# Kernel tuning notes

Hardware: AMD Instinct MI355X
Metric: run time of the kernel (lower is better)

Reference implementation:

```python
import jax, jax.numpy as jnp
import numpy as np

N_MEL = 80


def _bce_with_logits(x, t):
    # mean over all elements, numerically stable
    return jnp.mean(jnp.maximum(x, 0.0) - x * t + jnp.log1p(jnp.exp(-jnp.abs(x))))


def _spectral_mel_loss(pred, target):
    w = np.ones(N_MEL, dtype=np.float32)
    w[N_MEL // 4: 3 * N_MEL // 4] *= 1.5
    w[3 * N_MEL // 4:] *= 0.8
    w = jnp.asarray(w)[None, :, None]
    weighted_mse = jnp.mean((pred * w - target * w) ** 2)
    l1 = jnp.mean(jnp.abs(pred - target))
    dp = pred[:, :, 1:] - pred[:, :, :-1]
    dt = target[:, :, 1:] - target[:, :, :-1]
    spectral = jnp.mean((dp - dt) ** 2)
    return weighted_mse + 0.3 * l1 + 0.2 * spectral


def _perceptual_loss(pred, target):
    fw = jnp.exp(-jnp.arange(N_MEL, dtype=jnp.float32) / 20.0)[None, :, None]
    weighted = ((pred - target) ** 2) * fw
    l1 = jnp.mean(jnp.abs(pred - target))
    return jnp.mean(weighted) + 0.5 * l1


def _style_loss(pred, target):
    mean_loss = jnp.mean((jnp.mean(pred, axis=2) - jnp.mean(target, axis=2)) ** 2)
    # torch.var defaults to unbiased (ddof=1)
    var_loss = jnp.mean((jnp.var(pred, axis=2, ddof=1) - jnp.var(target, axis=2, ddof=1)) ** 2)
    c, t = pred.shape[1], pred.shape[2]
    gram_p = jnp.einsum('bct,bdt->bcd', pred, pred) / (c * t)
    gram_t = jnp.einsum('bct,bdt->bcd', target, target) / (c * t)
    gram_loss = jnp.mean((gram_p - gram_t) ** 2)
    return mean_loss + var_loss + 0.5 * gram_loss


def _monotonic_loss(att):
    # att: [B, mel_len, text_len]; vectorized form of the per-step violation loop
    b, mel_len, _ = att.shape
    peaks = jnp.argmax(att, axis=2).astype(jnp.float32)  # [B, mel_len]
    viol = jnp.maximum(peaks[:, :-1] - peaks[:, 1:], 0.0)
    return jnp.sum(viol) / (b * mel_len)


def setup_inputs() -> dict:
    key = jax.random.key(0)
    ks = jax.random.split(key, 6)
    B, C, T, L = 64, N_MEL, 2000, 200
    return {
        'mel_out': jax.random.normal(ks[0], (B, C, T), jnp.float32),
        'mel_out_postnet': jax.random.normal(ks[1], (B, C, T), jnp.float32),
        'mel_target': jax.random.normal(ks[2], (B, C, T), jnp.float32),
        'gate_out': jax.random.normal(ks[3], (B, T), jnp.float32),
        'gate_target': jax.random.uniform(ks[4], (B, T), jnp.float32),
        'attention_weights': jax.random.uniform(ks[5], (B, T, L), jnp.float32),
    }


def reference(mel_out, mel_out_postnet, mel_target, gate_out, gate_target, attention_weights):
    # loss weights (hparams defaults); guide_loss omitted (method truncated in source)
    mel_w, gate_w, spec_w, perc_w, style_w, mono_w = 1.0, 1.0, 0.3, 0.2, 0.1, 0.1
    gate_inner_w = 1.3  # AdaptiveGateLoss initial_weight

    mel_loss = jnp.mean((mel_out - mel_target) ** 2) + jnp.mean((mel_out_postnet - mel_target) ** 2)
    gate_loss = gate_inner_w * _bce_with_logits(gate_out.reshape(-1, 1), gate_target.reshape(-1, 1))
    spectral = _spectral_mel_loss(mel_out_postnet, mel_target)
    perceptual = _perceptual_loss(mel_out_postnet, mel_target)
    style = _style_loss(mel_out_postnet, mel_target)
    mono = _monotonic_loss(attention_weights)

    total = (mel_w * mel_loss + gate_w * gate_loss + spec_w * spectral
             + perc_w * perceptual + style_w * style + mono_w * mono)
    return total
```

## Files before the change

kernel.cpp:

```cpp
#include <hip/hip_runtime.h>
#include <math.h>

#define N_MEL 80
#define B_    64
#define T_    2000
#define L_    200
#define ROWS   (B_*N_MEL)
#define NTOT   (B_*N_MEL*T_)
#define GATE_N (B_*T_)
#define ATT_ROWS (B_*T_)

#define ACC_STRIDE 16
#define ACC_FLOATS 1024
#define VIOL_SLOT  16
#define WS_M8      ACC_FLOATS
#define WS_ROWPART (WS_M8 + 8*64*6400)

typedef __attribute__((ext_vector_type(8)))  short bf16x8;
typedef __attribute__((ext_vector_type(16))) float f32x16;

__device__ __forceinline__ float blockReduceSum256(float v) {
    __shared__ float red[4];
    #pragma unroll
    for (int off = 32; off; off >>= 1) v += __shfl_down(v, off, 64);
    int lane = threadIdx.x & 63, w = threadIdx.x >> 6;
    if (lane == 0) red[w] = v;
    __syncthreads();
    if (threadIdx.x == 0) v = red[0] + red[1] + red[2] + red[3];
    return v;
}

__device__ __forceinline__ unsigned short f2bf(float f) {
    unsigned u = __float_as_uint(f);
    u = (u + 0x7fffu + ((u >> 16) & 1u)) >> 16;
    return (unsigned short)u;
}

__global__ __launch_bounds__(256) void k_melrow(const float* __restrict__ mo,
                                                const float* __restrict__ mp,
                                                const float* __restrict__ mt,
                                                float* __restrict__ rowpart,
                                                float* __restrict__ acc) {
    if (blockIdx.x == 0) {
        *(float4*)(acc + threadIdx.x * 4) = make_float4(0.f, 0.f, 0.f, 0.f);
    }
    const int row = blockIdx.x;
    const long base = (long)row * T_;
    const float4* mo4 = (const float4*)(mo + base);
    const float4* mp4 = (const float4*)(mp + base);
    const float4* mt4 = (const float4*)(mt + base);

    float s1 = 0, s2 = 0, sl1 = 0, std_ = 0, sp = 0, sp2 = 0, st = 0, st2 = 0;
    for (int i = threadIdx.x; i < T_/4; i += 256) {
        float4 a = mo4[i], p = mp4[i], t = mt4[i];
        float e0 = a.x - t.x, e1 = a.y - t.y, e2 = a.z - t.z, e3 = a.w - t.w;
        s1 += e0*e0 + e1*e1 + e2*e2 + e3*e3;
        float d0 = p.x - t.x, d1 = p.y - t.y, d2 = p.z - t.z, d3 = p.w - t.w;
        s2 += d0*d0 + d1*d1 + d2*d2 + d3*d3;
        sl1 += fabsf(d0) + fabsf(d1) + fabsf(d2) + fabsf(d3);
        sp  += p.x + p.y + p.z + p.w;
        sp2 += p.x*p.x + p.y*p.y + p.z*p.z + p.w*p.w;
        st  += t.x + t.y + t.z + t.w;
        st2 += t.x*t.x + t.y*t.y + t.z*t.z + t.w*t.w;
        float q1 = d1 - d0, q2 = d2 - d1, q3 = d3 - d2;
        std_ += q1*q1 + q2*q2 + q3*q3;
        if (i > 0) {
            float dprev = mp[base + 4*i - 1] - mt[base + 4*i - 1];
            float q0 = d0 - dprev;
            std_ += q0*q0;
        }
    }

    __shared__ float red[4][8];
    float vals[8] = {s1, s2, sl1, std_, sp, sp2, st, st2};
    #pragma unroll
    for (int k = 0; k < 8; k++) {
        float v = vals[k];
        #pragma unroll
        for (int off = 32; off; off >>= 1) v += __shfl_down(v, off, 64);
        vals[k] = v;
    }
    int lane = threadIdx.x & 63, w = threadIdx.x >> 6;
    if (lane == 0) {
        #pragma unroll
        for (int k = 0; k < 8; k++) red[w][k] = vals[k];
    }
    __syncthreads();
    if (threadIdx.x == 0) {
        #pragma unroll
        for (int k = 0; k < 8; k++)
            rowpart[row*8 + k] = red[0][k] + red[1][k] + red[2][k] + red[3][k];
    }
}

__global__ __launch_bounds__(256) void k_melred(const float* __restrict__ rowpart,
                                                float* __restrict__ acc) {
    int row = blockIdx.x*256 + threadIdx.x;
    float a[8] = {0,0,0,0,0,0,0,0};
    if (row < ROWS) {
        const float4 lo = *(const float4*)(rowpart + row*8);
        const float4 hi = *(const float4*)(rowpart + row*8 + 4);
        float r0=lo.x, r1=lo.y, r2=lo.z, r3=lo.w, r4=hi.x, r5=hi.y, r6=hi.z, r7=hi.w;
        int c = row % N_MEL;
        float wc = (c >= 3*N_MEL/4) ? 0.8f : ((c >= N_MEL/4) ? 1.5f : 1.0f);
        float fw = expf(-(float)c / 20.0f);
        a[0] = r0;
        a[1] = r1;
        a[2] = wc*wc*r1;
        a[3] = r2;
        a[4] = r3;
        a[5] = fw*r1;
        float md = (r4 - r6) * (1.0f / T_);
        a[6] = md*md;
        float vp = (r5 - r4*r4*(1.0f/T_)) * (1.0f/(T_-1));
        float vt = (r7 - r6*r6*(1.0f/T_)) * (1.0f/(T_-1));
        float vd = vp - vt;
        a[7] = vd*vd;
    }
    __shared__ float red[4][8];
    #pragma unroll
    for (int k = 0; k < 8; k++) {
        float v = a[k];
        #pragma unroll
        for (int off = 32; off; off >>= 1) v += __shfl_down(v, off, 64);
        a[k] = v;
    }
    int lane = threadIdx.x & 63, w = threadIdx.x >> 6;
    if (lane == 0) {
        #pragma unroll
        for (int k = 0; k < 8; k++) red[w][k] = a[k];
    }
    __syncthreads();
    if (threadIdx.x == 0) {
        #pragma unroll
        for (int k = 0; k < 8; k++)
            atomicAdd(&acc[k*ACC_STRIDE], red[0][k] + red[1][k] + red[2][k] + red[3][k]);
    }
}

__global__ __launch_bounds__(256) void k_gate(const float* __restrict__ xp,
                                              const float* __restrict__ tp,
                                              float* __restrict__ acc) {
    const float4* x4 = (const float4*)xp;
    const float4* t4 = (const float4*)tp;
    float s = 0;
    for (int i = blockIdx.x*256 + threadIdx.x; i < GATE_N/4; i += gridDim.x*256) {
        float4 x = x4[i], t = t4[i];
        float xs[4] = {x.x, x.y, x.z, x.w}, ts[4] = {t.x, t.y, t.z, t.w};
        #pragma unroll
        for (int k = 0; k < 4; k++)
            s += fmaxf(xs[k], 0.0f) - xs[k]*ts[k] + log1pf(expf(-fabsf(xs[k])));
    }
    float tot = blockReduceSum256(s);
    if (threadIdx.x == 0) atomicAdd(&acc[8*ACC_STRIDE], tot);
}

#define AV_ROWS 64
__device__ __forceinline__ void scan_sub(const float* __restrict__ rowp, int q,
                                         float& bOut, int& pOut) {
    const float4* rp = (const float4*)rowp;
    float bx=-1.f, by=-1.f, bz=-1.f, bw=-1.f;
    int jx=0, jy=0, jz=0, jw=0;
    const int n = (q < 2) ? 13 : 12;
    #pragma unroll
    for (int i = 0; i < 13; i++) {
        if (i < n) {
            int j = q + 4*i;
            float4 v = rp[j];
            if (v.x > bx) { bx = v.x; jx = j; }
            if (v.y > by) { by = v.y; jy = j; }
            if (v.z > bz) { bz = v.z; jz = j; }
            if (v.w > bw) { bw = v.w; jw = j; }
        }
    }
    float b = bx; int p = 4*jx;
    if (by > b || (by == b && 4*jy+1 < p)) { b = by; p = 4*jy+1; }
    if (bz > b || (bz == b && 4*jz+2 < p)) { b = bz; p = 4*jz+2; }
    if (bw > b || (bw == b && 4*jw+3 < p)) { b = bw; p = 4*jw+3; }
    bOut = b; pOut = p;
}

__device__ __forceinline__ void merge4(float& b, int& p) {
    #pragma unroll
    for (int m = 1; m <= 2; m <<= 1) {
        float ob = __shfl_xor(b, m, 64);
        int   op = __shfl_xor(p, m, 64);
        if (ob > b || (ob == b && op < p)) { b = ob; p = op; }
    }
}

__global__ __launch_bounds__(256) void k_argviol(const float* __restrict__ att,
                                                 float* __restrict__ acc) {
    __shared__ float pk[AV_ROWS + 1];
    const int g = threadIdx.x >> 2;
    const int q = threadIdx.x & 3;
    const int r0 = blockIdx.x * AV_ROWS;
    const int r  = r0 + g;

    float b; int p;
    scan_sub(att + (long)r * L_, q, b, p);
    merge4(b, p);
    if (q == 0) pk[g] = (float)p;

    const int rb = r0 + AV_ROWS;
    const bool need_b = ((rb % T_) != 0) && (rb < ATT_ROWS);
    if (g == 0 && need_b) {
        float b2; int p2;
        scan_sub(att + (long)rb * L_, q, b2, p2);
        merge4(b2, p2);
        if (q == 0) pk[AV_ROWS] = (float)p2;
    }
    __syncthreads();

    float s = 0;
    if (threadIdx.x < AV_ROWS) {
        int rr = r0 + threadIdx.x;
        if (((rr + 1) % T_) != 0)
            s = fmaxf(pk[threadIdx.x] - pk[threadIdx.x + 1], 0.0f);
    }
    float tot = blockReduceSum256(s);
    if (threadIdx.x == 0)
        atomicAdd(&acc[(VIOL_SLOT + (blockIdx.x & 15))*ACC_STRIDE], tot);
}

__global__ __launch_bounds__(192) void k_gram(const float* __restrict__ mp,
                                              const float* __restrict__ mt,
                                              float* __restrict__ M8) {
    const int b  = blockIdx.x >> 3;
    const int kc = blockIdx.x & 7;
    const int k0 = kc * 256;
    const int NS = (kc < 7) ? 16 : 13;

    __shared__ unsigned short Dls[2][96][24];
    __shared__ unsigned short Sls[2][96][24];

    const int tid  = threadIdx.x;
    const int row  = tid >> 1;
    const int half = tid & 1;
    const int lane = tid & 63;
    const int wv   = tid >> 6;
    const long bbase = (long)b * (N_MEL * T_);
    const float* prow = mp + bbase + (long)row * T_ + k0 + half * 8;
    const float* trow = mt + bbase + (long)row * T_ + k0 + half * 8;
    const bool rv = (row < N_MEL);

    f32x16 acc0 = {}, acc1 = {}, acc2 = {};
    float4 pa0, pa1, ta0, ta1;

    auto loadreg = [&](int s) {
        if (rv) {
            pa0 = *(const float4*)(prow + s*16);
            pa1 = *(const float4*)(prow + s*16 + 4);
            ta0 = *(const float4*)(trow + s*16);
            ta1 = *(const float4*)(trow + s*16 + 4);
        } else {
            pa0 = pa1 = ta0 = ta1 = make_float4(0.f, 0.f, 0.f, 0.f);
        }
    };
    auto writelds = [&](int buf) {
        bf16x8 d, s;
        d[0]=f2bf(pa0.x-ta0.x); d[1]=f2bf(pa0.y-ta0.y); d[2]=f2bf(pa0.z-ta0.z); d[3]=f2bf(pa0.w-ta0.w);
        d[4]=f2bf(pa1.x-ta1.x); d[5]=f2bf(pa1.y-ta1.y); d[6]=f2bf(pa1.z-ta1.z); d[7]=f2bf(pa1.w-ta1.w);
        s[0]=f2bf(pa0.x+ta0.x); s[1]=f2bf(pa0.y+ta0.y); s[2]=f2bf(pa0.z+ta0.z); s[3]=f2bf(pa0.w+ta0.w);
        s[4]=f2bf(pa1.x+ta1.x); s[5]=f2bf(pa1.y+ta1.y); s[6]=f2bf(pa1.z+ta1.z); s[7]=f2bf(pa1.w+ta1.w);
        *(bf16x8*)&Dls[buf][row][half*8] = d;
        *(bf16x8*)&Sls[buf][row][half*8] = s;
    };

    loadreg(0);
    writelds(0);
    __syncthreads();

    const int frow = lane & 31;
    const int fkh  = lane >> 5;
    for (int s = 0; s < NS; s++) {
        const int cur = s & 1;
        if (s + 1 < NS) loadreg(s + 1);
        bf16x8 af = *(const bf16x8*)&Dls[cur][wv*32 + frow][fkh*8];
        bf16x8 b0 = *(const bf16x8*)&Sls[cur][      frow][fkh*8];
        bf16x8 b1 = *(const bf16x8*)&Sls[cur][ 32 + frow][fkh*8];
        bf16x8 b2 = *(const bf16x8*)&Sls[cur][ 64 + frow][fkh*8];
        acc0 = __builtin_amdgcn_mfma_f32_32x32x16_bf16(af, b0, acc0, 0, 0, 0);
        acc1 = __builtin_amdgcn_mfma_f32_32x32x16_bf16(af, b1, acc1, 0, 0, 0);
        acc2 = __builtin_amdgcn_mfma_f32_32x32x16_bf16(af, b2, acc2, 0, 0, 0);
        if (s + 1 < NS) writelds((s + 1) & 1);
        __syncthreads();
    }

    float* Mb = M8 + ((long)(kc * B_ + b)) * 6400;
    #pragma unroll
    for (int r = 0; r < 16; r++) {
        int row32 = (r & 3) + 8 * (r >> 2) + 4 * (lane >> 5);
        int c = wv * 32 + row32;
        if (c < N_MEL) {
            Mb[c*80 + frow]      = acc0[r];
            Mb[c*80 + 32 + frow] = acc1[r];
            if (frow < 16) Mb[c*80 + 64 + frow] = acc2[r];
        }
    }
}

__global__ __launch_bounds__(256) void k_gramfin(const float* __restrict__ M8,
                                                 float* __restrict__ acc) {
    __shared__ float Ms[N_MEL][N_MEL + 1];
    const int b = blockIdx.x;
    const float inv = 1.0f / (float)(N_MEL * T_);

    for (int i = threadIdx.x; i < 6400; i += 256) {
        float m = 0.f;
        #pragma unroll
        for (int kc = 0; kc < 8; kc++)
            m += M8[((long)(kc * B_ + b)) * 6400 + i];
        Ms[i / N_MEL][i % N_MEL] = m;
    }
    __syncthreads();

    float s = 0.f;
    for (int i = threadIdx.x; i < 6400; i += 256) {
        int c = i / N_MEL, d = i % N_MEL;
        float g = 0.5f * (Ms[c][d] + Ms[d][c]) * inv;
        s += g * g;
    }
    float tot = blockReduceSum256(s);
    if (threadIdx.x == 0) atomicAdd(&acc[10*ACC_STRIDE], tot);
}

__global__ void k_final(const float* __restrict__ acc, float* __restrict__ out) {
    if (threadIdx.x == 0 && blockIdx.x == 0) {
        const float invN = 1.0f / (float)NTOT;
        float viol = 0.f;
        #pragma unroll
        for (int j = 0; j < 16; j++) viol += acc[(VIOL_SLOT + j)*ACC_STRIDE];
        float mel        = (acc[0*ACC_STRIDE] + acc[1*ACC_STRIDE]) * invN;
        float gate       = 1.3f * acc[8*ACC_STRIDE] / (float)GATE_N;
        float wmse       = acc[2*ACC_STRIDE] * invN;
        float l1         = acc[3*ACC_STRIDE] * invN;
        float sdiff      = acc[4*ACC_STRIDE] / (float)(B_ * N_MEL * (T_ - 1));
        float spectral   = wmse + 0.3f*l1 + 0.2f*sdiff;
        float perceptual = acc[5*ACC_STRIDE]*invN + 0.5f*l1;
        float mean_loss  = acc[6*ACC_STRIDE] / (float)ROWS;
        float var_loss   = acc[7*ACC_STRIDE] / (float)ROWS;
        float gram       = acc[10*ACC_STRIDE] / (float)(B_ * 6400);
        float style      = mean_loss + var_loss + 0.5f*gram;
        float mono       = viol / (float)(B_ * T_);
        out[0] = mel + gate + 0.3f*spectral + 0.2f*perceptual + 0.1f*style + 0.1f*mono;
    }
}

extern "C" void kernel_launch(void* const* d_in, const int* in_sizes, int n_in,
                              void* d_out, int out_size, void* d_ws, size_t ws_size,
                              hipStream_t stream) {
    const float* mo  = (const float*)d_in[0];
    const float* mp  = (const float*)d_in[1];
    const float* mt  = (const float*)d_in[2];
    const float* gx  = (const float*)d_in[3];
    const float* gt  = (const float*)d_in[4];
    const float* att = (const float*)d_in[5];
    float* ws      = (float*)d_ws;
    float* acc     = ws;
    float* M8      = ws + WS_M8;
    float* rowpart = ws + WS_ROWPART;

    k_melrow <<<ROWS, 256, 0, stream>>>(mo, mp, mt, rowpart, acc);
    k_melred <<<20,   256, 0, stream>>>(rowpart, acc);
    k_gram   <<<512,  192, 0, stream>>>(mp, mt, M8);
    k_gramfin<<<64,   256, 0, stream>>>(M8, acc);
    k_gate   <<<64,   256, 0, stream>>>(gx, gt, acc);
    k_argviol<<<ATT_ROWS/AV_ROWS, 256, 0, stream>>>(att, acc);
    k_final  <<<1,    64,  0, stream>>>(acc, (float*)d_out);
}
```

Before: 92.97 us.

## Fuse mel, gram, argmax and gate kernels into one launch, drop atomics

Merges the four independent stage kernels (mel row stats, gram MFMA, attention argmax violations, gate BCE) into a single block-indexed mega-kernel, so they share one launch and can run concurrently instead of back to back. Global atomics into an accumulator are replaced by per-block partial slots, and the row reduction is moved into a single-block final kernel. This removes launch gaps and tail idle time. In exchange the gram blocks run with 256 threads where 64 are idle, and the final reduction is serialized in one block.

```diff
diff --git a/kernel.cpp b/kernel.cpp
--- a/kernel.cpp
+++ b/kernel.cpp
@@ -9,15 +9,23 @@
 #define NTOT   (B_*N_MEL*T_)
 #define GATE_N (B_*T_)
 #define ATT_ROWS (B_*T_)
-
-#define ACC_STRIDE 16
-#define ACC_FLOATS 1024
-#define VIOL_SLOT  16
-#define WS_M8      ACC_FLOATS
-#define WS_ROWPART (WS_M8 + 8*64*6400)
+#define AV_ROWS 64
+#define NVIOL  (ATT_ROWS/AV_ROWS)
+
+#define G_MELROW 5120
+#define G_GRAM   512
+#define G_ARGV   NVIOL
+#define G_GATE   64
+
+#define WS_ROWPART 0
+#define WS_M8      (WS_ROWPART + ROWS*8)
+#define WS_GATEP   (WS_M8 + 8*64*6400)
+#define WS_VIOLP   (WS_GATEP + 64)
+#define WS_GFP     (WS_VIOLP + NVIOL)
 
 typedef __attribute__((ext_vector_type(8)))  short bf16x8;
 typedef __attribute__((ext_vector_type(16))) float f32x16;
+typedef unsigned short ush;
 
 __device__ __forceinline__ float blockReduceSum256(float v) {
     __shared__ float red[4];
@@ -36,126 +44,6 @@
     return (unsigned short)u;
 }
 
-__global__ __launch_bounds__(256) void k_melrow(const float* __restrict__ mo,
-                                                const float* __restrict__ mp,
-                                                const float* __restrict__ mt,
-                                                float* __restrict__ rowpart,
-                                                float* __restrict__ acc) {
-    if (blockIdx.x == 0) {
-        *(float4*)(acc + threadIdx.x * 4) = make_float4(0.f, 0.f, 0.f, 0.f);
-    }
-    const int row = blockIdx.x;
-    const long base = (long)row * T_;
-    const float4* mo4 = (const float4*)(mo + base);
-    const float4* mp4 = (const float4*)(mp + base);
-    const float4* mt4 = (const float4*)(mt + base);
-
-    float s1 = 0, s2 = 0, sl1 = 0, std_ = 0, sp = 0, sp2 = 0, st = 0, st2 = 0;
-    for (int i = threadIdx.x; i < T_/4; i += 256) {
-        float4 a = mo4[i], p = mp4[i], t = mt4[i];
-        float e0 = a.x - t.x, e1 = a.y - t.y, e2 = a.z - t.z, e3 = a.w - t.w;
-        s1 += e0*e0 + e1*e1 + e2*e2 + e3*e3;
-        float d0 = p.x - t.x, d1 = p.y - t.y, d2 = p.z - t.z, d3 = p.w - t.w;
-        s2 += d0*d0 + d1*d1 + d2*d2 + d3*d3;
-        sl1 += fabsf(d0) + fabsf(d1) + fabsf(d2) + fabsf(d3);
-        sp  += p.x + p.y + p.z + p.w;
-        sp2 += p.x*p.x + p.y*p.y + p.z*p.z + p.w*p.w;
-        st  += t.x + t.y + t.z + t.w;
-        st2 += t.x*t.x + t.y*t.y + t.z*t.z + t.w*t.w;
-        float q1 = d1 - d0, q2 = d2 - d1, q3 = d3 - d2;
-        std_ += q1*q1 + q2*q2 + q3*q3;
-        if (i > 0) {
-            float dprev = mp[base + 4*i - 1] - mt[base + 4*i - 1];
-            float q0 = d0 - dprev;
-            std_ += q0*q0;
-        }
-    }
-
-    __shared__ float red[4][8];
-    float vals[8] = {s1, s2, sl1, std_, sp, sp2, st, st2};
-    #pragma unroll
-    for (int k = 0; k < 8; k++) {
-        float v = vals[k];
-        #pragma unroll
-        for (int off = 32; off; off >>= 1) v += __shfl_down(v, off, 64);
-        vals[k] = v;
-    }
-    int lane = threadIdx.x & 63, w = threadIdx.x >> 6;
-    if (lane == 0) {
-        #pragma unroll
-        for (int k = 0; k < 8; k++) red[w][k] = vals[k];
-    }
-    __syncthreads();
-    if (threadIdx.x == 0) {
-        #pragma unroll
-        for (int k = 0; k < 8; k++)
-            rowpart[row*8 + k] = red[0][k] + red[1][k] + red[2][k] + red[3][k];
-    }
-}
-
-__global__ __launch_bounds__(256) void k_melred(const float* __restrict__ rowpart,
-                                                float* __restrict__ acc) {
-    int row = blockIdx.x*256 + threadIdx.x;
-    float a[8] = {0,0,0,0,0,0,0,0};
-    if (row < ROWS) {
-        const float4 lo = *(const float4*)(rowpart + row*8);
-        const float4 hi = *(const float4*)(rowpart + row*8 + 4);
-        float r0=lo.x, r1=lo.y, r2=lo.z, r3=lo.w, r4=hi.x, r5=hi.y, r6=hi.z, r7=hi.w;
-        int c = row % N_MEL;
-        float wc = (c >= 3*N_MEL/4) ? 0.8f : ((c >= N_MEL/4) ? 1.5f : 1.0f);
-        float fw = expf(-(float)c / 20.0f);
-        a[0] = r0;
-        a[1] = r1;
-        a[2] = wc*wc*r1;
-        a[3] = r2;
-        a[4] = r3;
-        a[5] = fw*r1;
-        float md = (r4 - r6) * (1.0f / T_);
-        a[6] = md*md;
-        float vp = (r5 - r4*r4*(1.0f/T_)) * (1.0f/(T_-1));
-        float vt = (r7 - r6*r6*(1.0f/T_)) * (1.0f/(T_-1));
-        float vd = vp - vt;
-        a[7] = vd*vd;
-    }
-    __shared__ float red[4][8];
-    #pragma unroll
-    for (int k = 0; k < 8; k++) {
-        float v = a[k];
-        #pragma unroll
-        for (int off = 32; off; off >>= 1) v += __shfl_down(v, off, 64);
-        a[k] = v;
-    }
-    int lane = threadIdx.x & 63, w = threadIdx.x >> 6;
-    if (lane == 0) {
-        #pragma unroll
-        for (int k = 0; k < 8; k++) red[w][k] = a[k];
-    }
-    __syncthreads();
-    if (threadIdx.x == 0) {
-        #pragma unroll
-        for (int k = 0; k < 8; k++)
-            atomicAdd(&acc[k*ACC_STRIDE], red[0][k] + red[1][k] + red[2][k] + red[3][k]);
-    }
-}
-
-__global__ __launch_bounds__(256) void k_gate(const float* __restrict__ xp,
-                                              const float* __restrict__ tp,
-                                              float* __restrict__ acc) {
-    const float4* x4 = (const float4*)xp;
-    const float4* t4 = (const float4*)tp;
-    float s = 0;
-    for (int i = blockIdx.x*256 + threadIdx.x; i < GATE_N/4; i += gridDim.x*256) {
-        float4 x = x4[i], t = t4[i];
-        float xs[4] = {x.x, x.y, x.z, x.w}, ts[4] = {t.x, t.y, t.z, t.w};
-        #pragma unroll
-        for (int k = 0; k < 4; k++)
-            s += fmaxf(xs[k], 0.0f) - xs[k]*ts[k] + log1pf(expf(-fabsf(xs[k])));
-    }
-    float tot = blockReduceSum256(s);
-    if (threadIdx.x == 0) atomicAdd(&acc[8*ACC_STRIDE], tot);
-}
-
-#define AV_ROWS 64
 __device__ __forceinline__ void scan_sub(const float* __restrict__ rowp, int q,
                                          float& bOut, int& pOut) {
     const float4* rp = (const float4*)rowp;
@@ -189,120 +77,207 @@
     }
 }
 
-__global__ __launch_bounds__(256) void k_argviol(const float* __restrict__ att,
-                                                 float* __restrict__ acc) {
-    __shared__ float pk[AV_ROWS + 1];
-    const int g = threadIdx.x >> 2;
-    const int q = threadIdx.x & 3;
-    const int r0 = blockIdx.x * AV_ROWS;
-    const int r  = r0 + g;
-
-    float b; int p;
-    scan_sub(att + (long)r * L_, q, b, p);
-    merge4(b, p);
-    if (q == 0) pk[g] = (float)p;
-
-    const int rb = r0 + AV_ROWS;
-    const bool need_b = ((rb % T_) != 0) && (rb < ATT_ROWS);
-    if (g == 0 && need_b) {
-        float b2; int p2;
-        scan_sub(att + (long)rb * L_, q, b2, p2);
-        merge4(b2, p2);
-        if (q == 0) pk[AV_ROWS] = (float)p2;
-    }
-    __syncthreads();
-
-    float s = 0;
-    if (threadIdx.x < AV_ROWS) {
-        int rr = r0 + threadIdx.x;
-        if (((rr + 1) % T_) != 0)
-            s = fmaxf(pk[threadIdx.x] - pk[threadIdx.x + 1], 0.0f);
-    }
-    float tot = blockReduceSum256(s);
-    if (threadIdx.x == 0)
-        atomicAdd(&acc[(VIOL_SLOT + (blockIdx.x & 15))*ACC_STRIDE], tot);
-}
-
-__global__ __launch_bounds__(192) void k_gram(const float* __restrict__ mp,
+__global__ __launch_bounds__(256) void k_mega(const float* __restrict__ mo,
+                                              const float* __restrict__ mp,
                                               const float* __restrict__ mt,
-                                              float* __restrict__ M8) {
-    const int b  = blockIdx.x >> 3;
-    const int kc = blockIdx.x & 7;
-    const int k0 = kc * 256;
-    const int NS = (kc < 7) ? 16 : 13;
-
-    __shared__ unsigned short Dls[2][96][24];
-    __shared__ unsigned short Sls[2][96][24];
-
-    const int tid  = threadIdx.x;
-    const int row  = tid >> 1;
-    const int half = tid & 1;
-    const int lane = tid & 63;
-    const int wv   = tid >> 6;
-    const long bbase = (long)b * (N_MEL * T_);
-    const float* prow = mp + bbase + (long)row * T_ + k0 + half * 8;
-    const float* trow = mt + bbase + (long)row * T_ + k0 + half * 8;
-    const bool rv = (row < N_MEL);
-
-    f32x16 acc0 = {}, acc1 = {}, acc2 = {};
-    float4 pa0, pa1, ta0, ta1;
-
-    auto loadreg = [&](int s) {
-        if (rv) {
-            pa0 = *(const float4*)(prow + s*16);
-            pa1 = *(const float4*)(prow + s*16 + 4);
-            ta0 = *(const float4*)(trow + s*16);
-            ta1 = *(const float4*)(trow + s*16 + 4);
-        } else {
-            pa0 = pa1 = ta0 = ta1 = make_float4(0.f, 0.f, 0.f, 0.f);
-        }
-    };
-    auto writelds = [&](int buf) {
-        bf16x8 d, s;
-        d[0]=f2bf(pa0.x-ta0.x); d[1]=f2bf(pa0.y-ta0.y); d[2]=f2bf(pa0.z-ta0.z); d[3]=f2bf(pa0.w-ta0.w);
-        d[4]=f2bf(pa1.x-ta1.x); d[5]=f2bf(pa1.y-ta1.y); d[6]=f2bf(pa1.z-ta1.z); d[7]=f2bf(pa1.w-ta1.w);
-        s[0]=f2bf(pa0.x+ta0.x); s[1]=f2bf(pa0.y+ta0.y); s[2]=f2bf(pa0.z+ta0.z); s[3]=f2bf(pa0.w+ta0.w);
-        s[4]=f2bf(pa1.x+ta1.x); s[5]=f2bf(pa1.y+ta1.y); s[6]=f2bf(pa1.z+ta1.z); s[7]=f2bf(pa1.w+ta1.w);
-        *(bf16x8*)&Dls[buf][row][half*8] = d;
-        *(bf16x8*)&Sls[buf][row][half*8] = s;
-    };
-
-    loadreg(0);
-    writelds(0);
-    __syncthreads();
-
-    const int frow = lane & 31;
-    const int fkh  = lane >> 5;
-    for (int s = 0; s < NS; s++) {
-        const int cur = s & 1;
-        if (s + 1 < NS) loadreg(s + 1);
-        bf16x8 af = *(const bf16x8*)&Dls[cur][wv*32 + frow][fkh*8];
-        bf16x8 b0 = *(const bf16x8*)&Sls[cur][      frow][fkh*8];
-        bf16x8 b1 = *(const bf16x8*)&Sls[cur][ 32 + frow][fkh*8];
-        bf16x8 b2 = *(const bf16x8*)&Sls[cur][ 64 + frow][fkh*8];
-        acc0 = __builtin_amdgcn_mfma_f32_32x32x16_bf16(af, b0, acc0, 0, 0, 0);
-        acc1 = __builtin_amdgcn_mfma_f32_32x32x16_bf16(af, b1, acc1, 0, 0, 0);
-        acc2 = __builtin_amdgcn_mfma_f32_32x32x16_bf16(af, b2, acc2, 0, 0, 0);
-        if (s + 1 < NS) writelds((s + 1) & 1);
+                                              const float* __restrict__ gx,
+                                              const float* __restrict__ gt,
+                                              const float* __restrict__ att,
+                                              float* __restrict__ ws) {
+    __shared__ alignas(16) unsigned char smem[18432];
+    const int bid = blockIdx.x;
+    float* rowpart = ws + WS_ROWPART;
+    float* M8      = ws + WS_M8;
+    float* gatep   = ws + WS_GATEP;
+    float* violp   = ws + WS_VIOLP;
+
+    if (bid < G_MELROW) {
+        const int row = bid;
+        const long base = (long)row * T_;
+        const float4* mo4 = (const float4*)(mo + base);
+        const float4* mp4 = (const float4*)(mp + base);
+        const float4* mt4 = (const float4*)(mt + base);
+
+        float s1 = 0, s2 = 0, sl1 = 0, std_ = 0, sp = 0, sp2 = 0, st = 0, st2 = 0;
+        for (int i = threadIdx.x; i < T_/4; i += 256) {
+            float4 a = mo4[i], p = mp4[i], t = mt4[i];
+            float e0 = a.x - t.x, e1 = a.y - t.y, e2 = a.z - t.z, e3 = a.w - t.w;
+            s1 += e0*e0 + e1*e1 + e2*e2 + e3*e3;
+            float d0 = p.x - t.x, d1 = p.y - t.y, d2 = p.z - t.z, d3 = p.w - t.w;
+            s2 += d0*d0 + d1*d1 + d2*d2 + d3*d3;
+            sl1 += fabsf(d0) + fabsf(d1) + fabsf(d2) + fabsf(d3);
+            sp  += p.x + p.y + p.z + p.w;
+            sp2 += p.x*p.x + p.y*p.y + p.z*p.z + p.w*p.w;
+            st  += t.x + t.y + t.z + t.w;
+            st2 += t.x*t.x + t.y*t.y + t.z*t.z + t.w*t.w;
+            float q1 = d1 - d0, q2 = d2 - d1, q3 = d3 - d2;
+            std_ += q1*q1 + q2*q2 + q3*q3;
+            if (i > 0) {
+                float dprev = mp[base + 4*i - 1] - mt[base + 4*i - 1];
+                float q0 = d0 - dprev;
+                std_ += q0*q0;
+            }
+        }
+
+        float (*red)[8] = reinterpret_cast<float(*)[8]>(smem);
+        float vals[8] = {s1, s2, sl1, std_, sp, sp2, st, st2};
+        #pragma unroll
+        for (int k = 0; k < 8; k++) {
+            float v = vals[k];
+            #pragma unroll
+            for (int off = 32; off; off >>= 1) v += __shfl_down(v, off, 64);
+            vals[k] = v;
+        }
+        int lane = threadIdx.x & 63, w = threadIdx.x >> 6;
+        if (lane == 0) {
+            #pragma unroll
+            for (int k = 0; k < 8; k++) red[w][k] = vals[k];
+        }
         __syncthreads();
-    }
-
-    float* Mb = M8 + ((long)(kc * B_ + b)) * 6400;
-    #pragma unroll
-    for (int r = 0; r < 16; r++) {
-        int row32 = (r & 3) + 8 * (r >> 2) + 4 * (lane >> 5);
-        int c = wv * 32 + row32;
-        if (c < N_MEL) {
-            Mb[c*80 + frow]      = acc0[r];
-            Mb[c*80 + 32 + frow] = acc1[r];
-            if (frow < 16) Mb[c*80 + 64 + frow] = acc2[r];
-        }
-    }
-}
-
-__global__ __launch_bounds__(256) void k_gramfin(const float* __restrict__ M8,
-                                                 float* __restrict__ acc) {
+        if (threadIdx.x == 0) {
+            #pragma unroll
+            for (int k = 0; k < 8; k++)
+                rowpart[row*8 + k] = red[0][k] + red[1][k] + red[2][k] + red[3][k];
+        }
+        return;
+    }
+
+    if (bid < G_MELROW + G_GRAM) {
+        const int gb = bid - G_MELROW;
+        const int b  = gb >> 3;
+        const int kc = gb & 7;
+        const int k0 = kc * 256;
+        const int NS = (kc < 7) ? 16 : 13;
+
+        ush (*Dls)[96][24] = reinterpret_cast<ush(*)[96][24]>(smem);
+        ush (*Sls)[96][24] = reinterpret_cast<ush(*)[96][24]>(smem + 9216);
+
+        const int tid  = threadIdx.x;
+        const bool act = (tid < 192);
+        const int row  = tid >> 1;
+        const int half = tid & 1;
+        const int lane = tid & 63;
+        const int wv   = tid >> 6;
+        const long bbase = (long)b * (N_MEL * T_);
+        const float* prow = mp + bbase + (long)(row < 80 ? row : 0) * T_ + k0 + half * 8;
+        const float* trow = mt + bbase + (long)(row < 80 ? row : 0) * T_ + k0 + half * 8;
+        const bool rv = act && (row < N_MEL);
+
+        f32x16 acc0 = {}, acc1 = {}, acc2 = {};
+        float4 pa0, pa1, ta0, ta1;
+
+        auto loadreg = [&](int s) {
+            if (rv) {
+                pa0 = *(const float4*)(prow + s*16);
+                pa1 = *(const float4*)(prow + s*16 + 4);
+                ta0 = *(const float4*)(trow + s*16);
+                ta1 = *(const float4*)(trow + s*16 + 4);
+            } else {
+                pa0 = pa1 = ta0 = ta1 = make_float4(0.f, 0.f, 0.f, 0.f);
+            }
+        };
+        auto writelds = [&](int buf) {
+            bf16x8 d, s;
+            d[0]=f2bf(pa0.x-ta0.x); d[1]=f2bf(pa0.y-ta0.y); d[2]=f2bf(pa0.z-ta0.z); d[3]=f2bf(pa0.w-ta0.w);
+            d[4]=f2bf(pa1.x-ta1.x); d[5]=f2bf(pa1.y-ta1.y); d[6]=f2bf(pa1.z-ta1.z); d[7]=f2bf(pa1.w-ta1.w);
+            s[0]=f2bf(pa0.x+ta0.x); s[1]=f2bf(pa0.y+ta0.y); s[2]=f2bf(pa0.z+ta0.z); s[3]=f2bf(pa0.w+ta0.w);
+            s[4]=f2bf(pa1.x+ta1.x); s[5]=f2bf(pa1.y+ta1.y); s[6]=f2bf(pa1.z+ta1.z); s[7]=f2bf(pa1.w+ta1.w);
+            *(bf16x8*)&Dls[buf][row][half*8] = d;
+            *(bf16x8*)&Sls[buf][row][half*8] = s;
+        };
+
+        if (act) { loadreg(0); writelds(0); }
+        __syncthreads();
+
+        const int frow = lane & 31;
+        const int fkh  = lane >> 5;
+        for (int s = 0; s < NS; s++) {
+            const int cur = s & 1;
+            if (act) {
+                if (s + 1 < NS) loadreg(s + 1);
+                bf16x8 af = *(const bf16x8*)&Dls[cur][wv*32 + frow][fkh*8];
+                bf16x8 b0 = *(const bf16x8*)&Sls[cur][      frow][fkh*8];
+                bf16x8 b1 = *(const bf16x8*)&Sls[cur][ 32 + frow][fkh*8];
+                bf16x8 b2 = *(const bf16x8*)&Sls[cur][ 64 + frow][fkh*8];
+                acc0 = __builtin_amdgcn_mfma_f32_32x32x16_bf16(af, b0, acc0, 0, 0, 0);
+                acc1 = __builtin_amdgcn_mfma_f32_32x32x16_bf16(af, b1, acc1, 0, 0, 0);
+                acc2 = __builtin_amdgcn_mfma_f32_32x32x16_bf16(af, b2, acc2, 0, 0, 0);
+                if (s + 1 < NS) writelds((s + 1) & 1);
+            }
+            __syncthreads();
+        }
+
+        if (act) {
+            float* Mb = M8 + ((long)(kc * B_ + b)) * 6400;
+            #pragma unroll
+            for (int r = 0; r < 16; r++) {
+                int row32 = (r & 3) + 8 * (r >> 2) + 4 * (lane >> 5);
+                int c = wv * 32 + row32;
+                if (c < N_MEL) {
+                    Mb[c*80 + frow]      = acc0[r];
+                    Mb[c*80 + 32 + frow] = acc1[r];
+                    if (frow < 16) Mb[c*80 + 64 + frow] = acc2[r];
+                }
+            }
+        }
+        return;
+    }
+
+    if (bid < G_MELROW + G_GRAM + G_ARGV) {
+        const int ab = bid - (G_MELROW + G_GRAM);
+        float* pk = reinterpret_cast<float*>(smem);
+        const int g = threadIdx.x >> 2;
+        const int q = threadIdx.x & 3;
+        const int r0 = ab * AV_ROWS;
+        const int r  = r0 + g;
+
+        float b; int p;
+        scan_sub(att + (long)r * L_, q, b, p);
+        merge4(b, p);
+        if (q == 0) pk[g] = (float)p;
+
+        const int rb = r0 + AV_ROWS;
+        const bool need_b = ((rb % T_) != 0) && (rb < ATT_ROWS);
+        if (g == 0 && need_b) {
+            float b2; int p2;
+            scan_sub(att + (long)rb * L_, q, b2, p2);
+            merge4(b2, p2);
+            if (q == 0) pk[AV_ROWS] = (float)p2;
+        }
+        __syncthreads();
+
+        float s = 0;
+        if (threadIdx.x < AV_ROWS) {
+            int rr = r0 + threadIdx.x;
+            if (((rr + 1) % T_) != 0)
+                s = fmaxf(pk[threadIdx.x] - pk[threadIdx.x + 1], 0.0f);
+        }
+        float tot = blockReduceSum256(s);
+        if (threadIdx.x == 0) violp[ab] = tot;
+        return;
+    }
+
+    {
+        const int gb = bid - (G_MELROW + G_GRAM + G_ARGV);
+        const float4* x4 = (const float4*)gx;
+        const float4* t4 = (const float4*)gt;
+        float s = 0;
+        for (int i = gb*256 + threadIdx.x; i < GATE_N/4; i += G_GATE*256) {
+            float4 x = x4[i], t = t4[i];
+            float xs[4] = {x.x, x.y, x.z, x.w}, ts[4] = {t.x, t.y, t.z, t.w};
+            #pragma unroll
+            for (int k = 0; k < 4; k++)
+                s += fmaxf(xs[k], 0.0f) - xs[k]*ts[k] + log1pf(expf(-fabsf(xs[k])));
+        }
+        float tot = blockReduceSum256(s);
+        if (threadIdx.x == 0) gatep[gb] = tot;
+    }
+}
+
+__global__ __launch_bounds__(256) void k_gramfin(const float* __restrict__ ws_ro,
+                                                 float* __restrict__ gfp) {
     __shared__ float Ms[N_MEL][N_MEL + 1];
+    const float* M8 = ws_ro + WS_M8;
     const int b = blockIdx.x;
     const float inv = 1.0f / (float)(N_MEL * T_);
 
@@ -322,27 +297,70 @@
         s += g * g;
     }
     float tot = blockReduceSum256(s);
-    if (threadIdx.x == 0) atomicAdd(&acc[10*ACC_STRIDE], tot);
-}
-
-__global__ void k_final(const float* __restrict__ acc, float* __restrict__ out) {
-    if (threadIdx.x == 0 && blockIdx.x == 0) {
+    if (threadIdx.x == 0) gfp[b] = tot;
+}
+
+__global__ __launch_bounds__(256) void k_final2(const float* __restrict__ ws_ro,
+                                                float* __restrict__ out) {
+    const float* rowpart = ws_ro + WS_ROWPART;
+    const float* gatep   = ws_ro + WS_GATEP;
+    const float* violp   = ws_ro + WS_VIOLP;
+    const float* gfp     = ws_ro + WS_GFP;
+
+    float a[11] = {0,0,0,0,0,0,0,0,0,0,0};
+    for (int row = threadIdx.x; row < ROWS; row += 256) {
+        const float4 lo = *(const float4*)(rowpart + row*8);
+        const float4 hi = *(const float4*)(rowpart + row*8 + 4);
+        int c = row % N_MEL;
+        float wc = (c >= 3*N_MEL/4) ? 0.8f : ((c >= N_MEL/4) ? 1.5f : 1.0f);
+        float fw = expf(-(float)c / 20.0f);
+        a[0] += lo.x;
+        a[1] += lo.y;
+        a[2] += wc*wc*lo.y;
+        a[3] += lo.z;
+        a[4] += lo.w;
+        a[5] += fw*lo.y;
+        float md = (hi.x - hi.z) * (1.0f / T_);
+        a[6] += md*md;
+        float vp = (hi.y - hi.x*hi.x*(1.0f/T_)) * (1.0f/(T_-1));
+        float vt = (hi.w - hi.z*hi.z*(1.0f/T_)) * (1.0f/(T_-1));
+        float vd = vp - vt;
+        a[7] += vd*vd;
+    }
+    for (int i = threadIdx.x; i < NVIOL; i += 256) a[9] += violp[i];
+    if (threadIdx.x < 64) { a[8] = gatep[threadIdx.x]; a[10] = gfp[threadIdx.x]; }
+
+    __shared__ float red[4][11];
+    #pragma unroll
+    for (int k = 0; k < 11; k++) {
+        float v = a[k];
+        #pragma unroll
+        for (int off = 32; off; off >>= 1) v += __shfl_down(v, off, 64);
+        a[k] = v;
+    }
+    int lane = threadIdx.x & 63, w = threadIdx.x >> 6;
+    if (lane == 0) {
+        #pragma unroll
+        for (int k = 0; k < 11; k++) red[w][k] = a[k];
+    }
+    __syncthreads();
+    if (threadIdx.x == 0) {
+        float r[11];
+        #pragma unroll
+        for (int k = 0; k < 11; k++) r[k] = red[0][k] + red[1][k] + red[2][k] + red[3][k];
         const float invN = 1.0f / (float)NTOT;
-        float viol = 0.f;
-        #pragma unroll
-        for (int j = 0; j < 16; j++) viol += acc[(VIOL_SLOT + j)*ACC_STRIDE];
-        float mel        = (acc[0*ACC_STRIDE] + acc[1*ACC_STRIDE]) * invN;
-        float gate       = 1.3f * acc[8*ACC_STRIDE] / (float)GATE_N;
-        float wmse       = acc[2*ACC_STRIDE] * invN;
-        float l1         = acc[3*ACC_STRIDE] * invN;
-        float sdiff      = acc[4*ACC_STRIDE] / (float)(B_ * N_MEL * (T_ - 1));
+        float mel        = (r[0] + r[1]) * invN;
+        float gate       = 1.3f * r[8] / (float)GATE_N;
+        float wmse       = r[2] * invN;
+        float l1         = r[3] * invN;
+        float sdiff      = r[4] / (float)(B_ * N_MEL * (T_ - 1));
         float spectral   = wmse + 0.3f*l1 + 0.2f*sdiff;
-        float perceptual = acc[5*ACC_STRIDE]*invN + 0.5f*l1;
-        float mean_loss  = acc[6*ACC_STRIDE] / (float)ROWS;
-        float var_loss   = acc[7*ACC_STRIDE] / (float)ROWS;
-        float gram       = acc[10*ACC_STRIDE] / (float)(B_ * 6400);
+        float perceptual = r[5]*invN + 0.5f*l1;
+        float mean_loss  = r[6] / (float)ROWS;
+        float var_loss   = r[7] / (float)ROWS;
+        float gram       = r[10] / (float)(B_ * 6400);
         float style      = mean_loss + var_loss + 0.5f*gram;
-        float mono       = viol / (float)(B_ * T_);
+        float mono       = r[9] / (float)(B_ * T_);
         out[0] = mel + gate + 0.3f*spectral + 0.2f*perceptual + 0.1f*style + 0.1f*mono;
     }
 }
@@ -356,16 +374,10 @@
     const float* gx  = (const float*)d_in[3];
     const float* gt  = (const float*)d_in[4];
     const float* att = (const float*)d_in[5];
-    float* ws      = (float*)d_ws;
-    float* acc     = ws;
-    float* M8      = ws + WS_M8;
-    float* rowpart = ws + WS_ROWPART;
-
-    k_melrow <<<ROWS, 256, 0, stream>>>(mo, mp, mt, rowpart, acc);
-    k_melred <<<20,   256, 0, stream>>>(rowpart, acc);
-    k_gram   <<<512,  192, 0, stream>>>(mp, mt, M8);
-    k_gramfin<<<64,   256, 0, stream>>>(M8, acc);
-    k_gate   <<<64,   256, 0, stream>>>(gx, gt, acc);
-    k_argviol<<<ATT_ROWS/AV_ROWS, 256, 0, stream>>>(att, acc);
-    k_final  <<<1,    64,  0, stream>>>(acc, (float*)d_out);
-}
+    float* ws = (float*)d_ws;
+
+    const int g1 = G_MELROW + G_GRAM + G_ARGV + G_GATE;
+    k_mega   <<<g1, 256, 0, stream>>>(mo, mp, mt, gx, gt, att, ws);
+    k_gramfin<<<64, 256, 0, stream>>>(ws, ws + WS_GFP);
+    k_final2 <<<1,  256, 0, stream>>>(ws, (float*)d_out);
+}
```

After: 89.04 us (median of 2 runs). -4.2%, faster.
